# Optimization experiments

Hardware: AMD Instinct MI355X
Metric: run time of the kernel (lower is better)

The kernel has to match this reference:

```python
import jax, jax.numpy as jnp
import numpy as np

B, CLIP, P, E, H = 1024, 1024, 32, 2048, 16  # batch, clip_dim, prefix_length, token_emb_dim, num_heads
DH = E // H  # head dim = 128


def setup_inputs() -> dict:
    key = jax.random.key(0)
    ks = jax.random.split(key, 8)
    w = lambda k, sh: (jax.random.normal(k, sh, jnp.float32) * 0.02)
    return {
        "image_embs": jax.random.normal(ks[0], (B, CLIP), jnp.float32),
        "Wm": w(ks[1], (E, CLIP)),           # memory_proj weight
        "bm": jnp.zeros((E,), jnp.float32),
        "prefix_queries": w(ks[2], (P, E)),   # learned prefix queries
        "Win": w(ks[3], (3 * E, E)),          # MHA packed in_proj weight [q;k;v]
        "bin": jnp.zeros((3 * E,), jnp.float32),
        "Wo_mha": w(ks[4], (E, E)),           # MHA out_proj
        "bo_mha": jnp.zeros((E,), jnp.float32),
        "Wo": w(ks[5], (E, E)),               # adapter out_proj
        "bo": jnp.zeros((E,), jnp.float32),
    }


def reference(image_embs, Wm, bm, prefix_queries, Win, bin, Wo_mha, bo_mha, Wo, bo):
    Bn = image_embs.shape[0]
    # memory_proj: (B, clip_dim) -> (B, E); memory seq length is 1
    mem = image_embs @ Wm.T + bm
    # packed q/k/v projections, as in nn.MultiheadAttention
    Wq, Wk, Wv = Win[:E], Win[E:2 * E], Win[2 * E:]
    bq, bk, bv = bin[:E], bin[E:2 * E], bin[2 * E:]
    q = prefix_queries @ Wq.T + bq          # (P, E), shared across batch (queries are expanded)
    k = mem @ Wk.T + bk                     # (B, E)
    v = mem @ Wv.T + bv                     # (B, E)
    qh = q.reshape(P, H, DH)                # (P, H, dh)
    kh = k.reshape(Bn, H, DH)               # (B, H, dh)
    vh = v.reshape(Bn, H, DH)               # (B, H, dh)
    # scaled dot-product attention with kv_len = 1
    scores = jnp.einsum("phd,bhd->bhp", qh, kh) / jnp.sqrt(jnp.float32(DH))  # (B, H, P)
    attn = jax.nn.softmax(scores[..., None], axis=-1)  # (B, H, P, 1); trivially all-ones
    attn_out = jnp.einsum("bhpk,bhkd->bphd", attn, vh[:, :, None, :])  # (B, P, H, dh)
    attn_out = attn_out.reshape(Bn, P, E)
    out = attn_out @ Wo_mha.T + bo_mha      # MHA out_proj
    out = out @ Wo.T + bo                   # adapter out_proj
    return out
```

## Files before the change

### kernel.cpp

```cpp
#include <hip/hip_runtime.h>


#define BM 64
#define BN 64
#define BK 64
#define NA 5

typedef __attribute__((ext_vector_type(8))) __bf16 bf16x8;
typedef __attribute__((ext_vector_type(8))) unsigned short u16x8;
typedef __attribute__((ext_vector_type(4))) float f32x4;

__device__ __forceinline__ unsigned short f2bf(float f) {
  unsigned int u = __float_as_uint(f);
  u += 0x7FFFu + ((u >> 16) & 1u);
  return (unsigned short)(u >> 16);
}

__device__ __forceinline__ u16x8 cvt8(float4 v0, float4 v1) {
  u16x8 o;
  o[0] = f2bf(v0.x); o[1] = f2bf(v0.y); o[2] = f2bf(v0.z); o[3] = f2bf(v0.w);
  o[4] = f2bf(v1.x); o[5] = f2bf(v1.y); o[6] = f2bf(v1.z); o[7] = f2bf(v1.w);
  return o;
}

template <int KLOG2>
__device__ __forceinline__ void pack_w8(const float* __restrict__ src,
                                        unsigned short* __restrict__ dst,
                                        size_t u) {
  const size_t n = u >> (KLOG2 - 3);
  const size_t ko = u & (((size_t)1 << (KLOG2 - 3)) - 1);
  const float4 v0 = reinterpret_cast<const float4*>(src)[u * 2];
  const float4 v1 = reinterpret_cast<const float4*>(src)[u * 2 + 1];
  const size_t frag = (n >> 4) * ((size_t)1 << (KLOG2 - 5)) + (ko >> 2);
  const size_t lane = ((ko & 3) << 4) + (n & 15);
  reinterpret_cast<u16x8*>(dst)[frag * 64 + lane] = cvt8(v0, v1);
}

__device__ __forceinline__ void gload_lds16(const void* g, void* l) {
  __builtin_amdgcn_global_load_lds(
      (const __attribute__((address_space(1))) void*)g,
      (__attribute__((address_space(3))) void*)l, 16, 0, 0);
}

__global__ __launch_bounds__(256) void cvt_xw(const float* __restrict__ x,
                                              const float* __restrict__ wm,
                                              unsigned short* __restrict__ xb,
                                              unsigned short* __restrict__ wmb) {
  size_t u = (size_t)blockIdx.x * 256 + threadIdx.x;
  for (; u < 393216; u += 262144) {
    if (u < 131072) {
      const float4 v0 = reinterpret_cast<const float4*>(x)[u * 2];
      const float4 v1 = reinterpret_cast<const float4*>(x)[u * 2 + 1];
      reinterpret_cast<u16x8*>(xb)[u] = cvt8(v0, v1);
    } else {
      pack_w8<10>(wm, wmb, u - 131072);
    }
  }
}

template <int NT, int EPI, bool CVT>
__global__ __launch_bounds__(256, 2) void gemm_bt(
    const unsigned short* __restrict__ A, const unsigned short* __restrict__ Wp,
    const float* __restrict__ bias, void* __restrict__ outp,
    const float* __restrict__ cvt_src, unsigned short* __restrict__ cvt_dst,
    int cvt_nu) {
  __shared__ __attribute__((aligned(16))) unsigned short As[NA][BM * BK];
  const int tid = threadIdx.x;
  const int lane = tid & 63;
  const int wid = tid >> 6;
  const int rm = (wid >> 1) * 32;
  const int cn = (wid & 1) * 32;
  const int bid = blockIdx.x;
  const int bn0 = ((bid & 7) * 4 + (bid >> 7)) * BN;
  const int bm0 = ((bid >> 3) & 15) * BM;
  const int l15 = lane & 15;
  const int l4 = lane >> 4;
  const int lr = lane >> 3;
  const int lc = lane & 7;
  const int scol = ((lc ^ lr) << 3);
  const int KT = NT * 2;
  const size_t Kz = (size_t)(NT * 64);

  f32x4 acc[2][2] = {};
  bf16x8 breg[4][2][2];
  const unsigned short* wlane = Wp + lane * 8;
  const int fb_n = ((bn0 + cn) >> 4);

  auto stageA = [&](int buf, int tile) {
    const int k0 = tile * BK;
#pragma unroll
    for (int j = 0; j < 2; ++j) {
      const int c = wid * 2 + j;
      gload_lds16(A + (size_t)(bm0 + c * 8 + lr) * Kz + (k0 + scol),
                  &As[buf][c * 512]);
    }
  };

  auto loadB = [&](int slot, int tile) {
#pragma unroll
    for (int ni = 0; ni < 2; ++ni)
#pragma unroll
      for (int ks = 0; ks < 2; ++ks) {
        const size_t frag = (size_t)(fb_n + ni) * KT + tile * 2 + ks;
        breg[slot][ni][ks] =
            *reinterpret_cast<const bf16x8*>(wlane + frag * 512);
      }
  };

  auto compute = [&](int buf, int slot) {
    const int swz = (l15 & 7) << 3;
#pragma unroll
    for (int ks = 0; ks < 2; ++ks) {
      const int kidx = (ks * 32 + l4 * 8) ^ swz;
      bf16x8 a[2];
#pragma unroll
      for (int mi = 0; mi < 2; ++mi)
        a[mi] = *reinterpret_cast<const bf16x8*>(
            &As[buf][(rm + mi * 16 + l15) * 64 + kidx]);
#pragma unroll
      for (int mi = 0; mi < 2; ++mi)
#pragma unroll
        for (int ni = 0; ni < 2; ++ni)
          acc[mi][ni] = __builtin_amdgcn_mfma_f32_16x16x32_bf16(
              a[mi], breg[slot][ni][ks], acc[mi][ni], 0, 0, 0);
    }
  };

#pragma unroll
  for (int p = 0; p < 3; ++p) { stageA(p, p); loadB(p, p); }
#pragma unroll
  for (int t = 0; t < NT; ++t) {
    if (t + 3 < NT) { stageA((t + 3) % NA, t + 3); loadB((t + 3) & 3, t + 3); }
    const int rem = NT - 1 - t;
    if (rem >= 3)      asm volatile("s_waitcnt vmcnt(18)" ::: "memory");
    else if (rem == 2) asm volatile("s_waitcnt vmcnt(12)" ::: "memory");
    else if (rem == 1) asm volatile("s_waitcnt vmcnt(6)" ::: "memory");
    else               asm volatile("s_waitcnt vmcnt(0)" ::: "memory");
    asm volatile("s_waitcnt lgkmcnt(0)" ::: "memory");
    __builtin_amdgcn_s_barrier();
    compute(t % NA, t & 3);
  }

  if (EPI == 0) {
#pragma unroll
    for (int mi = 0; mi < 2; ++mi)
#pragma unroll
      for (int ni = 0; ni < 2; ++ni) {
        const int col = bn0 + cn + ni * 16 + l15;
        const float bcol = bias[col];
#pragma unroll
        for (int i = 0; i < 4; ++i) {
          const int row = bm0 + rm + mi * 16 + l4 * 4 + i;
          ((unsigned short*)outp)[(size_t)row * 2048 + col] =
              f2bf(acc[mi][ni][i] + bcol);
        }
      }
  } else {
    asm volatile("s_waitcnt lgkmcnt(0)" ::: "memory");
    __builtin_amdgcn_s_barrier();
    float* Cs = (float*)As;
#pragma unroll
    for (int mi = 0; mi < 2; ++mi)
#pragma unroll
      for (int ni = 0; ni < 2; ++ni) {
        const int col = cn + ni * 16 + l15;
        const float bcol = bias[bn0 + col];
#pragma unroll
        for (int i = 0; i < 4; ++i)
          Cs[(rm + mi * 16 + l4 * 4 + i) * 68 + col] = acc[mi][ni][i] + bcol;
      }
    asm volatile("s_waitcnt lgkmcnt(0)" ::: "memory");
    __builtin_amdgcn_s_barrier();
    float* outf = (float*)outp;
    const int c4 = (lane & 15) * 4;
    const int psub = lane >> 4;
#pragma unroll
    for (int it = 0; it < 16; ++it) {
      const int rl = wid * 16 + it;
      const f32x4 v = *reinterpret_cast<const f32x4*>(&Cs[rl * 68 + c4]);
      float* ob = outf + ((size_t)(bm0 + rl) * 32 + psub) * 2048 + bn0 + c4;
#pragma unroll
      for (int pb = 0; pb < 8; ++pb)
        __builtin_nontemporal_store(
            v, reinterpret_cast<f32x4*>(ob + (size_t)pb * 4 * 2048));
    }
  }

  if (CVT) {
    size_t u = (size_t)bid * 256 + tid;
    for (; u < (size_t)cvt_nu; u += 131072) pack_w8<11>(cvt_src, cvt_dst, u);
  }
}

extern "C" void kernel_launch(void* const* d_in, const int* in_sizes, int n_in,
                              void* d_out, int out_size, void* d_ws, size_t ws_size,
                              hipStream_t stream) {
  const float* image = (const float*)d_in[0];
  const float* Wm   = (const float*)d_in[1];
  const float* bm   = (const float*)d_in[2];
  const float* Win  = (const float*)d_in[4];
  const float* bin  = (const float*)d_in[5];
  const float* Wo1  = (const float*)d_in[6];
  const float* bo1  = (const float*)d_in[7];
  const float* Wo2  = (const float*)d_in[8];
  const float* bo2  = (const float*)d_in[9];
  float* out = (float*)d_out;

  const float* Wv = Win + (size_t)2 * 2048 * 2048;
  const float* bv = bin + 2 * 2048;

  unsigned short* wsb = (unsigned short*)d_ws;
  unsigned short* Xb   = wsb;
  unsigned short* Wmb  = wsb + (1u << 20);
  unsigned short* Wvb  = wsb + (3u << 20);
  unsigned short* W1b  = wsb + (7u << 20);
  unsigned short* W2b  = wsb + (11u << 20);
  unsigned short* act0 = wsb + (15u << 20);
  unsigned short* act1 = wsb + (17u << 20);
  unsigned short* act2 = wsb + (19u << 20);

  cvt_xw<<<1024, 256, 0, stream>>>(image, Wm, Xb, Wmb);

  gemm_bt<16, 0, true><<<512, 256, 0, stream>>>(Xb, Wmb, bm, act0,
                                                Wv, Wvb, 524288);
  gemm_bt<32, 0, true><<<512, 256, 0, stream>>>(act0, Wvb, bv, act1,
                                                Wo1, W1b, 524288);
  gemm_bt<32, 0, true><<<512, 256, 0, stream>>>(act1, W1b, bo1, act2,
                                                Wo2, W2b, 524288);
  gemm_bt<32, 1, false><<<512, 256, 0, stream>>>(act2, W2b, bo2, out,
                                                 nullptr, nullptr, 0);
  (void)n_in; (void)in_sizes; (void)out_size; (void)ws_size;
}
```

Measured before the change: 132.7 us.

## Load A operands directly from fragment-packed layout into registers, drop LDS staging

The activations and the input matrix are now stored in the same MFMA-fragment-packed layout as the weights. Each GEMM can then load A fragments straight from global memory into registers, like B, instead of going through swizzled LDS buffers with manual waitcnt and barriers. The bf16 epilogue goes through a small LDS tile and writes its output in this packed layout for the next GEMM. LDS use is smaller and launch bounds rise to 3 blocks per CU, in exchange for more register pressure and more global traffic for A, since A fragments are no longer shared across waves through LDS.

```diff
diff --git a/kernel.cpp b/kernel.cpp
--- a/kernel.cpp
+++ b/kernel.cpp
@@ -4,7 +4,6 @@
 #define BM 64
 #define BN 64
 #define BK 64
-#define NA 5
 
 typedef __attribute__((ext_vector_type(8))) __bf16 bf16x8;
 typedef __attribute__((ext_vector_type(8))) unsigned short u16x8;
@@ -27,19 +26,13 @@
 __device__ __forceinline__ void pack_w8(const float* __restrict__ src,
                                         unsigned short* __restrict__ dst,
                                         size_t u) {
-  const size_t n = u >> (KLOG2 - 3);
+  const size_t r = u >> (KLOG2 - 3);
   const size_t ko = u & (((size_t)1 << (KLOG2 - 3)) - 1);
   const float4 v0 = reinterpret_cast<const float4*>(src)[u * 2];
   const float4 v1 = reinterpret_cast<const float4*>(src)[u * 2 + 1];
-  const size_t frag = (n >> 4) * ((size_t)1 << (KLOG2 - 5)) + (ko >> 2);
-  const size_t lane = ((ko & 3) << 4) + (n & 15);
+  const size_t frag = (r >> 4) * ((size_t)1 << (KLOG2 - 5)) + (ko >> 2);
+  const size_t lane = ((ko & 3) << 4) + (r & 15);
   reinterpret_cast<u16x8*>(dst)[frag * 64 + lane] = cvt8(v0, v1);
-}
-
-__device__ __forceinline__ void gload_lds16(const void* g, void* l) {
-  __builtin_amdgcn_global_load_lds(
-      (const __attribute__((address_space(1))) void*)g,
-      (__attribute__((address_space(3))) void*)l, 16, 0, 0);
 }
 
 __global__ __launch_bounds__(256) void cvt_xw(const float* __restrict__ x,
@@ -48,23 +41,18 @@
                                               unsigned short* __restrict__ wmb) {
   size_t u = (size_t)blockIdx.x * 256 + threadIdx.x;
   for (; u < 393216; u += 262144) {
-    if (u < 131072) {
-      const float4 v0 = reinterpret_cast<const float4*>(x)[u * 2];
-      const float4 v1 = reinterpret_cast<const float4*>(x)[u * 2 + 1];
-      reinterpret_cast<u16x8*>(xb)[u] = cvt8(v0, v1);
-    } else {
-      pack_w8<10>(wm, wmb, u - 131072);
-    }
+    if (u < 131072) pack_w8<10>(x, xb, u);
+    else            pack_w8<10>(wm, wmb, u - 131072);
   }
 }
 
 template <int NT, int EPI, bool CVT>
-__global__ __launch_bounds__(256, 2) void gemm_bt(
+__global__ __launch_bounds__(256, 3) void gemm_bt(
     const unsigned short* __restrict__ A, const unsigned short* __restrict__ Wp,
     const float* __restrict__ bias, void* __restrict__ outp,
     const float* __restrict__ cvt_src, unsigned short* __restrict__ cvt_dst,
     int cvt_nu) {
-  __shared__ __attribute__((aligned(16))) unsigned short As[NA][BM * BK];
+  __shared__ __attribute__((aligned(16))) float Csh[64 * 68];
   const int tid = threadIdx.x;
   const int lane = tid & 63;
   const int wid = tid >> 6;
@@ -75,90 +63,56 @@
   const int bm0 = ((bid >> 3) & 15) * BM;
   const int l15 = lane & 15;
   const int l4 = lane >> 4;
-  const int lr = lane >> 3;
-  const int lc = lane & 7;
-  const int scol = ((lc ^ lr) << 3);
   const int KT = NT * 2;
-  const size_t Kz = (size_t)(NT * 64);
+  const int fa = (bm0 + rm) >> 4;
+  const int fb = (bn0 + cn) >> 4;
 
   f32x4 acc[2][2] = {};
-  bf16x8 breg[4][2][2];
+  bf16x8 areg[4][2][2], breg[4][2][2];
+  const unsigned short* alane = A + lane * 8;
   const unsigned short* wlane = Wp + lane * 8;
-  const int fb_n = ((bn0 + cn) >> 4);
-
-  auto stageA = [&](int buf, int tile) {
-    const int k0 = tile * BK;
-#pragma unroll
-    for (int j = 0; j < 2; ++j) {
-      const int c = wid * 2 + j;
-      gload_lds16(A + (size_t)(bm0 + c * 8 + lr) * Kz + (k0 + scol),
-                  &As[buf][c * 512]);
-    }
+
+  auto loadA = [&](int slot, int tile) {
+#pragma unroll
+    for (int mi = 0; mi < 2; ++mi)
+#pragma unroll
+      for (int ks = 0; ks < 2; ++ks)
+        areg[slot][mi][ks] = *reinterpret_cast<const bf16x8*>(
+            alane + ((size_t)(fa + mi) * KT + tile * 2 + ks) * 512);
   };
-
   auto loadB = [&](int slot, int tile) {
 #pragma unroll
     for (int ni = 0; ni < 2; ++ni)
 #pragma unroll
-      for (int ks = 0; ks < 2; ++ks) {
-        const size_t frag = (size_t)(fb_n + ni) * KT + tile * 2 + ks;
-        breg[slot][ni][ks] =
-            *reinterpret_cast<const bf16x8*>(wlane + frag * 512);
-      }
+      for (int ks = 0; ks < 2; ++ks)
+        breg[slot][ni][ks] = *reinterpret_cast<const bf16x8*>(
+            wlane + ((size_t)(fb + ni) * KT + tile * 2 + ks) * 512);
   };
-
-  auto compute = [&](int buf, int slot) {
-    const int swz = (l15 & 7) << 3;
-#pragma unroll
-    for (int ks = 0; ks < 2; ++ks) {
-      const int kidx = (ks * 32 + l4 * 8) ^ swz;
-      bf16x8 a[2];
-#pragma unroll
-      for (int mi = 0; mi < 2; ++mi)
-        a[mi] = *reinterpret_cast<const bf16x8*>(
-            &As[buf][(rm + mi * 16 + l15) * 64 + kidx]);
+  auto compute = [&](int slot) {
+#pragma unroll
+    for (int ks = 0; ks < 2; ++ks)
 #pragma unroll
       for (int mi = 0; mi < 2; ++mi)
 #pragma unroll
         for (int ni = 0; ni < 2; ++ni)
           acc[mi][ni] = __builtin_amdgcn_mfma_f32_16x16x32_bf16(
-              a[mi], breg[slot][ni][ks], acc[mi][ni], 0, 0, 0);
+              areg[slot][mi][ks], breg[slot][ni][ks], acc[mi][ni], 0, 0, 0);
+  };
+
+  loadA(0, 0); loadB(0, 0);
+  loadA(1, 1); loadB(1, 1);
+  loadA(2, 2); loadB(2, 2);
+#pragma unroll
+  for (int t = 0; t < NT; ++t) {
+    if (t + 3 < NT) {
+      loadA((t + 3) & 3, t + 3);
+      loadB((t + 3) & 3, t + 3);
     }
-  };
-
-#pragma unroll
-  for (int p = 0; p < 3; ++p) { stageA(p, p); loadB(p, p); }
-#pragma unroll
-  for (int t = 0; t < NT; ++t) {
-    if (t + 3 < NT) { stageA((t + 3) % NA, t + 3); loadB((t + 3) & 3, t + 3); }
-    const int rem = NT - 1 - t;
-    if (rem >= 3)      asm volatile("s_waitcnt vmcnt(18)" ::: "memory");
-    else if (rem == 2) asm volatile("s_waitcnt vmcnt(12)" ::: "memory");
-    else if (rem == 1) asm volatile("s_waitcnt vmcnt(6)" ::: "memory");
-    else               asm volatile("s_waitcnt vmcnt(0)" ::: "memory");
-    asm volatile("s_waitcnt lgkmcnt(0)" ::: "memory");
-    __builtin_amdgcn_s_barrier();
-    compute(t % NA, t & 3);
+    compute(t & 3);
   }
 
   if (EPI == 0) {
-#pragma unroll
-    for (int mi = 0; mi < 2; ++mi)
-#pragma unroll
-      for (int ni = 0; ni < 2; ++ni) {
-        const int col = bn0 + cn + ni * 16 + l15;
-        const float bcol = bias[col];
-#pragma unroll
-        for (int i = 0; i < 4; ++i) {
-          const int row = bm0 + rm + mi * 16 + l4 * 4 + i;
-          ((unsigned short*)outp)[(size_t)row * 2048 + col] =
-              f2bf(acc[mi][ni][i] + bcol);
-        }
-      }
-  } else {
-    asm volatile("s_waitcnt lgkmcnt(0)" ::: "memory");
-    __builtin_amdgcn_s_barrier();
-    float* Cs = (float*)As;
+    unsigned short* Cb = (unsigned short*)Csh;
 #pragma unroll
     for (int mi = 0; mi < 2; ++mi)
 #pragma unroll
@@ -167,17 +121,37 @@
         const float bcol = bias[bn0 + col];
 #pragma unroll
         for (int i = 0; i < 4; ++i)
-          Cs[(rm + mi * 16 + l4 * 4 + i) * 68 + col] = acc[mi][ni][i] + bcol;
+          Cb[(rm + mi * 16 + l4 * 4 + i) * 72 + col] =
+              f2bf(acc[mi][ni][i] + bcol);
       }
-    asm volatile("s_waitcnt lgkmcnt(0)" ::: "memory");
-    __builtin_amdgcn_s_barrier();
+    __syncthreads();
+    unsigned short* op = (unsigned short*)outp;
+#pragma unroll
+    for (int ktl = 0; ktl < 2; ++ktl) {
+      const u16x8 v = *reinterpret_cast<const u16x8*>(
+          &Cb[(wid * 16 + l15) * 72 + ktl * 32 + l4 * 8]);
+      const size_t unit = (size_t)(bm0 / 16 + wid) * 64 + bn0 / 32 + ktl;
+      *reinterpret_cast<u16x8*>(op + unit * 512 + lane * 8) = v;
+    }
+  } else {
+#pragma unroll
+    for (int mi = 0; mi < 2; ++mi)
+#pragma unroll
+      for (int ni = 0; ni < 2; ++ni) {
+        const int col = cn + ni * 16 + l15;
+        const float bcol = bias[bn0 + col];
+#pragma unroll
+        for (int i = 0; i < 4; ++i)
+          Csh[(rm + mi * 16 + l4 * 4 + i) * 68 + col] = acc[mi][ni][i] + bcol;
+      }
+    __syncthreads();
     float* outf = (float*)outp;
     const int c4 = (lane & 15) * 4;
     const int psub = lane >> 4;
 #pragma unroll
     for (int it = 0; it < 16; ++it) {
       const int rl = wid * 16 + it;
-      const f32x4 v = *reinterpret_cast<const f32x4*>(&Cs[rl * 68 + c4]);
+      const f32x4 v = *reinterpret_cast<const f32x4*>(&Csh[rl * 68 + c4]);
       float* ob = outf + ((size_t)(bm0 + rl) * 32 + psub) * 2048 + bn0 + c4;
 #pragma unroll
       for (int pb = 0; pb < 8; ++pb)
```

New measurement: 161.4 us. 21.6% more time.
